# Optimization experiments

Hardware: AMD Instinct MI355X
Metric: run time of the kernel (lower is better)

Reference implementation:

```python
import jax, jax.numpy as jnp
import numpy as np

N_EMBD = 1024
HEAD_SIZE = 64
B, T = 16, 2048


def setup_inputs() -> dict:
    key = jax.random.key(0)
    ks = jax.random.split(key, 7)
    s = 1.0 / np.sqrt(N_EMBD)
    return {
        "x": jax.random.normal(ks[0], (B, T, N_EMBD), dtype=jnp.float32),
        "Wq": jax.random.uniform(ks[1], (N_EMBD, HEAD_SIZE), jnp.float32, -s, s),
        "bq": jax.random.uniform(ks[2], (HEAD_SIZE,), jnp.float32, -s, s),
        "Wk": jax.random.uniform(ks[3], (N_EMBD, HEAD_SIZE), jnp.float32, -s, s),
        "bk": jax.random.uniform(ks[4], (HEAD_SIZE,), jnp.float32, -s, s),
        "Wv": jax.random.uniform(ks[5], (N_EMBD, HEAD_SIZE), jnp.float32, -s, s),
        "bv": jax.random.uniform(ks[6], (HEAD_SIZE,), jnp.float32, -s, s),
    }


def reference(x, Wq, bq, Wk, bk, Wv, bv):
    # x: [B, T, C]
    q = x @ Wq + bq          # [B, T, H]
    k = x @ Wk + bk          # [B, T, H]
    v = x @ Wv + bv          # [B, T, H]
    scale = k.shape[-1] ** -0.5
    wei = jnp.einsum("bth,bsh->bts", q, k) * scale  # [B, T, T]
    Tn = x.shape[1]
    causal = jnp.tril(jnp.ones((Tn, Tn), dtype=bool))
    wei = jnp.where(causal, wei, -jnp.inf)
    wei = jax.nn.softmax(wei, axis=-1)
    # dropout is identity in eval mode
    return jnp.einsum("bts,bsh->bth", wei, v)  # [B, T, H]
```

## Files before the change

### kernel.cpp

```cpp
#include <hip/hip_runtime.h>
#include <math.h>

#define BB 16
#define TT 2048
#define CC 1024
#define HH 64
#define MTOT (BB*TT)

typedef _Float16 f16;
typedef _Float16 f16x8 __attribute__((ext_vector_type(8)));
typedef float f32x4 __attribute__((ext_vector_type(4)));

#define WT_OFF 0
#define Q_OFF  196608
#define K_OFF  (Q_OFF + (size_t)MTOT*HH)
#define VT_OFF (K_OFF + (size_t)MTOT*HH)

__device__ __forceinline__ void async16(const void* g, void* l) {
    __builtin_amdgcn_global_load_lds(
        (const __attribute__((address_space(1))) unsigned int*)g,
        (__attribute__((address_space(3))) unsigned int*)l, 16, 0, 0);
}

__device__ __forceinline__ f16x8 cvt8(float4 u, float4 v) {
    f16x8 r;
    r[0] = (f16)u.x; r[1] = (f16)u.y; r[2] = (f16)u.z; r[3] = (f16)u.w;
    r[4] = (f16)v.x; r[5] = (f16)v.y; r[6] = (f16)v.z; r[7] = (f16)v.w;
    return r;
}

__global__ __launch_bounds__(256) void prep_kernel(
    const float* __restrict__ Wq, const float* __restrict__ Wk,
    const float* __restrict__ Wv, f16* __restrict__ ws)
{
    int e = blockIdx.x * 256 + threadIdx.x;
    int ng = e >> 10, k = e & 1023;
    int which = ng >> 6, n = ng & 63;
    const float* W = (which == 0) ? Wq : (which == 1) ? Wk : Wv;
    ws[WT_OFF + e] = (f16)W[k * HH + n];
}

__global__ __launch_bounds__(256, 2) void qkv_kernel(
    const float* __restrict__ x,
    const float* __restrict__ bq, const float* __restrict__ bk,
    const float* __restrict__ bv, f16* __restrict__ ws)
{
    __shared__ __align__(16) float Xs[64 * 64];
    __shared__ __align__(16) f16   Ws[192 * 64];
    __shared__ __align__(16) f16   Vt[64][72];

    const f16* wt = ws + WT_OFF;
    const int tid  = threadIdx.x;
    const int lane = tid & 63, w = tid >> 6;
    const int c = lane & 15, g = lane >> 4;
    const int m0 = blockIdx.x * 64;

    f32x4 acc[4][3];
    #pragma unroll
    for (int mt = 0; mt < 4; ++mt)
        #pragma unroll
        for (int j = 0; j < 3; ++j) acc[mt][j] = (f32x4){0.f, 0.f, 0.f, 0.f};

    for (int k0 = 0; k0 < CC; k0 += 64) {
        __syncthreads();
        #pragma unroll
        for (int i = 0; i < 4; ++i) {
            int G0 = (w * 4 + i) * 64;
            int G = G0 + lane;
            int r = G >> 4, q = G & 15;
            async16(x + (size_t)(m0 + r) * CC + k0 + ((q ^ (r & 15)) << 2),
                    Xs + G0 * 4);
        }
        #pragma unroll
        for (int i = 0; i < 6; ++i) {
            int G0 = (w * 6 + i) * 64;
            int G = G0 + lane;
            int r = G >> 3, q = G & 7;
            async16(wt + (size_t)r * CC + k0 + ((q ^ (r & 7)) << 3),
                    Ws + G0 * 8);
        }
        __syncthreads();

        #pragma unroll
        for (int kk = 0; kk < 2; ++kk) {
            f16x8 bfr[3];
            #pragma unroll
            for (int j = 0; j < 3; ++j) {
                int r = (3 * w + j) * 16 + c;
                int p = (kk * 4 + g) ^ (c & 7);
                bfr[j] = *(const f16x8*)(Ws + r * 64 + p * 8);
            }
            #pragma unroll
            for (int mt = 0; mt < 4; ++mt) {
                int r = mt * 16 + c;
                int q = kk * 8 + 2 * g;
                float4 f0 = *(const float4*)(Xs + r * 64 + (q ^ c) * 4);
                float4 f1 = *(const float4*)(Xs + r * 64 + ((q + 1) ^ c) * 4);
                f16x8 a = cvt8(f0, f1);
                #pragma unroll
                for (int j = 0; j < 3; ++j)
                    acc[mt][j] = __builtin_amdgcn_mfma_f32_16x16x32_f16(
                        a, bfr[j], acc[mt][j], 0, 0, 0);
            }
        }
    }

    #pragma unroll
    for (int j = 0; j < 3; ++j) {
        int nt = 3 * w + j;
        int plane = nt >> 2;
        int h = (nt & 3) * 16 + c;
        if (plane == 0) {
            float bias = bq[h];
            #pragma unroll
            for (int mt = 0; mt < 4; ++mt)
                #pragma unroll
                for (int r = 0; r < 4; ++r) {
                    int m = m0 + mt * 16 + 4 * g + r;
                    ws[Q_OFF + (size_t)m * HH + h] =
                        (f16)((acc[mt][j][r] + bias) * 0.125f);
                }
        } else if (plane == 1) {
            float bias = bk[h];
            #pragma unroll
            for (int mt = 0; mt < 4; ++mt)
                #pragma unroll
                for (int r = 0; r < 4; ++r) {
                    int m = m0 + mt * 16 + 4 * g + r;
                    ws[K_OFF + (size_t)m * HH + h] = (f16)(acc[mt][j][r] + bias);
                }
        } else {
            float bias = bv[h];
            #pragma unroll
            for (int mt = 0; mt < 4; ++mt)
                #pragma unroll
                for (int r = 0; r < 4; ++r)
                    Vt[h][mt * 16 + 4 * g + r] = (f16)(acc[mt][j][r] + bias);
        }
    }
    __syncthreads();
    {
        int h = tid >> 2, seg = tid & 3;
        f16* dst = ws + VT_OFF + (size_t)h * MTOT + m0 + seg * 16;
        *(f16x8*)dst       = *(f16x8*)&Vt[h][seg * 16];
        *(f16x8*)(dst + 8) = *(f16x8*)&Vt[h][seg * 16 + 8];
    }
}

__global__ __launch_bounds__(256, 2) void attn_kernel(
    const f16* __restrict__ ws, float* __restrict__ out)
{
    const f16* qp = ws + Q_OFF;
    const f16* kp = ws + K_OFF;
    const f16* vt = ws + VT_OFF;

    __shared__ __align__(16) f16 Qs[64 * 64];
    __shared__ __align__(16) f16 Ks[64 * 64];
    __shared__ __align__(16) f16 Vs[64 * 64];
    __shared__ __align__(16) f16 Ps[4][16][72];

    const int tid  = threadIdx.x;
    const int lane = tid & 63, w = tid >> 6;
    const int c = lane & 15, g = lane >> 4;

    const int id = blockIdx.x;
    const int r8 = id & 7, j = id >> 3;
    const int half = j >> 5, qr = j & 31;
    const int b  = 2 * r8 + half;
    const int qi = half ? (31 - qr) : qr;
    const int q0 = qi * 64;
    const size_t rowbase = (size_t)b * TT;

    #pragma unroll
    for (int i = 0; i < 2; ++i) {
        int G0 = (w * 2 + i) * 64;
        int G = G0 + lane;
        int r = G >> 3, q = G & 7;
        async16(qp + (rowbase + q0 + r) * HH + ((q ^ (r & 7)) << 3),
                Qs + G0 * 8);
    }

    f32x4 o[5];
    #pragma unroll
    for (int nt = 0; nt < 5; ++nt) o[nt] = (f32x4){0.f, 0.f, 0.f, 0.f};

    f16x8 onesf;
    #pragma unroll
    for (int i = 0; i < 8; ++i) onesf[i] = (c == 0) ? (f16)1.0f : (f16)0.0f;

    for (int st = 0; st <= qi; ++st) {
        const int s0 = st * 64;
        __syncthreads();
        #pragma unroll
        for (int i = 0; i < 2; ++i) {
            int G0 = (w * 2 + i) * 64;
            int G = G0 + lane;
            int r = G >> 3, q = G & 7;
            int sw = (q ^ (r & 7)) << 3;
            async16(kp + (rowbase + s0 + r) * HH + sw, Ks + G0 * 8);
            async16(vt + (size_t)r * MTOT + rowbase + s0 + sw, Vs + G0 * 8);
        }
        __syncthreads();

        f16x8 aq[2];
        {
            int r = w * 16 + c;
            aq[0] = *(const f16x8*)(Qs + r * 64 + ((g)     ^ (c & 7)) * 8);
            aq[1] = *(const f16x8*)(Qs + r * 64 + ((4 + g) ^ (c & 7)) * 8);
        }

        f32x4 s[4];
        #pragma unroll
        for (int nt = 0; nt < 4; ++nt) {
            s[nt] = (f32x4){0.f, 0.f, 0.f, 0.f};
            int r = nt * 16 + c;
            f16x8 b0 = *(const f16x8*)(Ks + r * 64 + ((g)     ^ (c & 7)) * 8);
            f16x8 b1 = *(const f16x8*)(Ks + r * 64 + ((4 + g) ^ (c & 7)) * 8);
            s[nt] = __builtin_amdgcn_mfma_f32_16x16x32_f16(aq[0], b0, s[nt], 0, 0, 0);
            s[nt] = __builtin_amdgcn_mfma_f32_16x16x32_f16(aq[1], b1, s[nt], 0, 0, 0);
        }

        if (st == qi) {
            #pragma unroll
            for (int nt = 0; nt < 4; ++nt)
                #pragma unroll
                for (int rr = 0; rr < 4; ++rr)
                    if (nt * 16 + c > w * 16 + 4 * g + rr) s[nt][rr] = -INFINITY;
        }

        #pragma unroll
        for (int nt = 0; nt < 4; ++nt)
            #pragma unroll
            for (int rr = 0; rr < 4; ++rr)
                Ps[w][4 * g + rr][nt * 16 + c] = (f16)__expf(s[nt][rr]);
        f16x8 pa0 = *(f16x8*)&Ps[w][c][g * 8];
        f16x8 pa1 = *(f16x8*)&Ps[w][c][32 + g * 8];

        #pragma unroll
        for (int nt = 0; nt < 4; ++nt) {
            int r = nt * 16 + c;
            f16x8 v0 = *(const f16x8*)(Vs + r * 64 + ((g)     ^ (c & 7)) * 8);
            f16x8 v1 = *(const f16x8*)(Vs + r * 64 + ((4 + g) ^ (c & 7)) * 8);
            o[nt] = __builtin_amdgcn_mfma_f32_16x16x32_f16(pa0, v0, o[nt], 0, 0, 0);
            o[nt] = __builtin_amdgcn_mfma_f32_16x16x32_f16(pa1, v1, o[nt], 0, 0, 0);
        }
        o[4] = __builtin_amdgcn_mfma_f32_16x16x32_f16(pa0, onesf, o[4], 0, 0, 0);
        o[4] = __builtin_amdgcn_mfma_f32_16x16x32_f16(pa1, onesf, o[4], 0, 0, 0);
    }

    #pragma unroll
    for (int rr = 0; rr < 4; ++rr) {
        float lv = __shfl(o[4][rr], lane & 48);
        float inv = 1.0f / lv;
        int mrow = q0 + w * 16 + 4 * g + rr;
        #pragma unroll
        for (int nt = 0; nt < 4; ++nt)
            out[(rowbase + mrow) * HH + nt * 16 + c] = o[nt][rr] * inv;
    }
}

extern "C" void kernel_launch(void* const* d_in, const int* in_sizes, int n_in,
                              void* d_out, int out_size, void* d_ws, size_t ws_size,
                              hipStream_t stream) {
    const float* x  = (const float*)d_in[0];
    const float* Wq = (const float*)d_in[1];
    const float* bq = (const float*)d_in[2];
    const float* Wk = (const float*)d_in[3];
    const float* bk = (const float*)d_in[4];
    const float* Wv = (const float*)d_in[5];
    const float* bv = (const float*)d_in[6];
    f16*   ws  = (f16*)d_ws;
    float* out = (float*)d_out;

    prep_kernel<<<768, 256, 0, stream>>>(Wq, Wk, Wv, ws);
    qkv_kernel<<<MTOT / 64, 256, 0, stream>>>(x, bq, bk, bv, ws);
    dim3 g2(512);
    attn_kernel<<<g2, 256, 0, stream>>>(ws, out);
}
```

Before: 241.0 us.

## Double-buffer K/V tiles and compute transposed scores in attention kernel

The attention kernel now double-buffers K and V tiles in LDS, prefetching the next tile asynchronously while computing the current one. It computes S^T with K as the A operand and Q held in registers, which removes the Q shared-memory tile. The row sum is accumulated with shuffles instead of an extra ones-vector MFMA, and MFMAs on fully masked diagonal sub-tiles are skipped. The QKV kernel reuses the X staging buffer for the V transpose, and both kernels raise their occupancy hint to 3 blocks, at the cost of more register pressure.

```diff
diff --git a/kernel.cpp b/kernel.cpp
--- a/kernel.cpp
+++ b/kernel.cpp
@@ -8,6 +8,7 @@
 #define MTOT (BB*TT)
 
 typedef _Float16 f16;
+typedef _Float16 f16x4 __attribute__((ext_vector_type(4)));
 typedef _Float16 f16x8 __attribute__((ext_vector_type(8)));
 typedef float f32x4 __attribute__((ext_vector_type(4)));
 
@@ -40,14 +41,14 @@
     ws[WT_OFF + e] = (f16)W[k * HH + n];
 }
 
-__global__ __launch_bounds__(256, 2) void qkv_kernel(
+__global__ __launch_bounds__(256, 3) void qkv_kernel(
     const float* __restrict__ x,
     const float* __restrict__ bq, const float* __restrict__ bk,
     const float* __restrict__ bv, f16* __restrict__ ws)
 {
     __shared__ __align__(16) float Xs[64 * 64];
     __shared__ __align__(16) f16   Ws[192 * 64];
-    __shared__ __align__(16) f16   Vt[64][72];
+    f16 (*Vt)[72] = (f16 (*)[72])Xs;
 
     const f16* wt = ws + WT_OFF;
     const int tid  = threadIdx.x;
@@ -104,6 +105,7 @@
             }
         }
     }
+    __syncthreads();
 
     #pragma unroll
     for (int j = 0; j < 3; ++j) {
@@ -147,17 +149,16 @@
     }
 }
 
-__global__ __launch_bounds__(256, 2) void attn_kernel(
+__global__ __launch_bounds__(256, 3) void attn_kernel(
     const f16* __restrict__ ws, float* __restrict__ out)
 {
     const f16* qp = ws + Q_OFF;
     const f16* kp = ws + K_OFF;
     const f16* vt = ws + VT_OFF;
 
-    __shared__ __align__(16) f16 Qs[64 * 64];
-    __shared__ __align__(16) f16 Ks[64 * 64];
-    __shared__ __align__(16) f16 Vs[64 * 64];
-    __shared__ __align__(16) f16 Ps[4][16][72];
+    __shared__ __align__(16) f16 Ks[2][64 * 64];
+    __shared__ __align__(16) f16 Vs[2][64 * 64];
+    __shared__ __align__(16) f16 PsT[4][16][68];
 
     const int tid  = threadIdx.x;
     const int lane = tid & 63, w = tid >> 6;
@@ -171,91 +172,89 @@
     const int q0 = qi * 64;
     const size_t rowbase = (size_t)b * TT;
 
-    #pragma unroll
-    for (int i = 0; i < 2; ++i) {
-        int G0 = (w * 2 + i) * 64;
-        int G = G0 + lane;
-        int r = G >> 3, q = G & 7;
-        async16(qp + (rowbase + q0 + r) * HH + ((q ^ (r & 7)) << 3),
-                Qs + G0 * 8);
-    }
-
-    f32x4 o[5];
-    #pragma unroll
-    for (int nt = 0; nt < 5; ++nt) o[nt] = (f32x4){0.f, 0.f, 0.f, 0.f};
-
-    f16x8 onesf;
-    #pragma unroll
-    for (int i = 0; i < 8; ++i) onesf[i] = (c == 0) ? (f16)1.0f : (f16)0.0f;
+    f16x8 bq_[2];
+    {
+        const f16* qrow = qp + (rowbase + q0 + w * 16 + c) * HH + g * 8;
+        bq_[0] = *(const f16x8*)(qrow);
+        bq_[1] = *(const f16x8*)(qrow + 32);
+    }
+
+    f32x4 o[4];
+    #pragma unroll
+    for (int ht = 0; ht < 4; ++ht) o[ht] = (f32x4){0.f, 0.f, 0.f, 0.f};
+    float l_acc = 0.f;
+
+    #define STAGE_KV(st) do {                                              \
+        int buf = (st) & 1;                                                \
+        _Pragma("unroll")                                                  \
+        for (int i = 0; i < 2; ++i) {                                      \
+            int G0 = (w * 2 + i) * 64;                                     \
+            int G = G0 + lane;                                             \
+            int r = G >> 3, q = G & 7;                                     \
+            int sw = (q ^ (r & 7)) << 3;                                   \
+            async16(kp + (rowbase + (st) * 64 + r) * HH + sw, &Ks[buf][G0 * 8]); \
+            async16(vt + (size_t)r * MTOT + rowbase + (st) * 64 + sw, &Vs[buf][G0 * 8]); \
+        }                                                                  \
+    } while (0)
+
+    STAGE_KV(0);
 
     for (int st = 0; st <= qi; ++st) {
-        const int s0 = st * 64;
         __syncthreads();
-        #pragma unroll
-        for (int i = 0; i < 2; ++i) {
-            int G0 = (w * 2 + i) * 64;
-            int G = G0 + lane;
-            int r = G >> 3, q = G & 7;
-            int sw = (q ^ (r & 7)) << 3;
-            async16(kp + (rowbase + s0 + r) * HH + sw, Ks + G0 * 8);
-            async16(vt + (size_t)r * MTOT + rowbase + s0 + sw, Vs + G0 * 8);
-        }
-        __syncthreads();
-
-        f16x8 aq[2];
-        {
-            int r = w * 16 + c;
-            aq[0] = *(const f16x8*)(Qs + r * 64 + ((g)     ^ (c & 7)) * 8);
-            aq[1] = *(const f16x8*)(Qs + r * 64 + ((4 + g) ^ (c & 7)) * 8);
-        }
-
-        f32x4 s[4];
-        #pragma unroll
-        for (int nt = 0; nt < 4; ++nt) {
-            s[nt] = (f32x4){0.f, 0.f, 0.f, 0.f};
-            int r = nt * 16 + c;
-            f16x8 b0 = *(const f16x8*)(Ks + r * 64 + ((g)     ^ (c & 7)) * 8);
-            f16x8 b1 = *(const f16x8*)(Ks + r * 64 + ((4 + g) ^ (c & 7)) * 8);
-            s[nt] = __builtin_amdgcn_mfma_f32_16x16x32_f16(aq[0], b0, s[nt], 0, 0, 0);
-            s[nt] = __builtin_amdgcn_mfma_f32_16x16x32_f16(aq[1], b1, s[nt], 0, 0, 0);
-        }
-
-        if (st == qi) {
-            #pragma unroll
-            for (int nt = 0; nt < 4; ++nt)
-                #pragma unroll
-                for (int rr = 0; rr < 4; ++rr)
-                    if (nt * 16 + c > w * 16 + 4 * g + rr) s[nt][rr] = -INFINITY;
-        }
-
-        #pragma unroll
-        for (int nt = 0; nt < 4; ++nt)
-            #pragma unroll
-            for (int rr = 0; rr < 4; ++rr)
-                Ps[w][4 * g + rr][nt * 16 + c] = (f16)__expf(s[nt][rr]);
-        f16x8 pa0 = *(f16x8*)&Ps[w][c][g * 8];
-        f16x8 pa1 = *(f16x8*)&Ps[w][c][32 + g * 8];
-
-        #pragma unroll
-        for (int nt = 0; nt < 4; ++nt) {
-            int r = nt * 16 + c;
-            f16x8 v0 = *(const f16x8*)(Vs + r * 64 + ((g)     ^ (c & 7)) * 8);
-            f16x8 v1 = *(const f16x8*)(Vs + r * 64 + ((4 + g) ^ (c & 7)) * 8);
-            o[nt] = __builtin_amdgcn_mfma_f32_16x16x32_f16(pa0, v0, o[nt], 0, 0, 0);
-            o[nt] = __builtin_amdgcn_mfma_f32_16x16x32_f16(pa1, v1, o[nt], 0, 0, 0);
-        }
-        o[4] = __builtin_amdgcn_mfma_f32_16x16x32_f16(pa0, onesf, o[4], 0, 0, 0);
-        o[4] = __builtin_amdgcn_mfma_f32_16x16x32_f16(pa1, onesf, o[4], 0, 0, 0);
-    }
-
-    #pragma unroll
-    for (int rr = 0; rr < 4; ++rr) {
-        float lv = __shfl(o[4][rr], lane & 48);
-        float inv = 1.0f / lv;
-        int mrow = q0 + w * 16 + 4 * g + rr;
-        #pragma unroll
-        for (int nt = 0; nt < 4; ++nt)
-            out[(rowbase + mrow) * HH + nt * 16 + c] = o[nt][rr] * inv;
+        if (st < qi) STAGE_KV(st + 1);
+        const f16* kb = Ks[st & 1];
+        const f16* vb = Vs[st & 1];
+        const int tmax = (st == qi) ? w : 3;
+        const bool diag = (st == qi);
+
+        float lp = 0.f;
+        #pragma unroll
+        for (int t = 0; t < 4; ++t) {
+            f16x4 pv;
+            if (t <= tmax) {
+                int r = t * 16 + c;
+                f16x8 a0 = *(const f16x8*)(kb + r * 64 + (((g)     ^ (c & 7)) << 3));
+                f16x8 a1 = *(const f16x8*)(kb + r * 64 + (((4 + g) ^ (c & 7)) << 3));
+                f32x4 s = (f32x4){0.f, 0.f, 0.f, 0.f};
+                s = __builtin_amdgcn_mfma_f32_16x16x32_f16(a0, bq_[0], s, 0, 0, 0);
+                s = __builtin_amdgcn_mfma_f32_16x16x32_f16(a1, bq_[1], s, 0, 0, 0);
+                #pragma unroll
+                for (int rr = 0; rr < 4; ++rr) {
+                    float p = (diag && t == w && (4 * g + rr > c))
+                                ? 0.f : __expf(s[rr]);
+                    lp += p;
+                    pv[rr] = (f16)p;
+                }
+            } else {
+                pv = (f16x4){(f16)0.f, (f16)0.f, (f16)0.f, (f16)0.f};
+            }
+            *(f16x4*)&PsT[w][c][t * 16 + 4 * g] = pv;
+        }
+        lp += __shfl_xor(lp, 16);
+        lp += __shfl_xor(lp, 32);
+        l_acc += lp;
+
+        f16x8 pb0 = *(const f16x8*)&PsT[w][c][g * 8];
+        f16x8 pb1 = *(const f16x8*)&PsT[w][c][32 + g * 8];
+        #pragma unroll
+        for (int ht = 0; ht < 4; ++ht) {
+            int r = ht * 16 + c;
+            f16x8 va0 = *(const f16x8*)(vb + r * 64 + (((g)     ^ (c & 7)) << 3));
+            f16x8 va1 = *(const f16x8*)(vb + r * 64 + (((4 + g) ^ (c & 7)) << 3));
+            o[ht] = __builtin_amdgcn_mfma_f32_16x16x32_f16(va0, pb0, o[ht], 0, 0, 0);
+            o[ht] = __builtin_amdgcn_mfma_f32_16x16x32_f16(va1, pb1, o[ht], 0, 0, 0);
+        }
+    }
+    #undef STAGE_KV
+
+    float inv = 1.0f / l_acc;
+    float* orow = out + (rowbase + q0 + w * 16 + c) * HH;
+    #pragma unroll
+    for (int ht = 0; ht < 4; ++ht) {
+        float4 v;
+        v.x = o[ht][0] * inv; v.y = o[ht][1] * inv;
+        v.z = o[ht][2] * inv; v.w = o[ht][3] * inv;
+        *(float4*)(orow + ht * 16 + 4 * g) = v;
     }
 }
 
@@ -274,6 +273,5 @@
 
     prep_kernel<<<768, 256, 0, stream>>>(Wq, Wk, Wv, ws);
     qkv_kernel<<<MTOT / 64, 256, 0, stream>>>(x, bq, bk, bv, ws);
-    dim3 g2(512);
-    attn_kernel<<<g2, 256, 0, stream>>>(ws, out);
-}
+    attn_kernel<<<512, 256, 0, stream>>>(ws, out);
+}
```

Result: no change. 245.5 us (+1.8%).
